# Performance work log

Hardware: AMD Instinct MI355X
Metric: run time of the kernel (lower is better)

Reference implementation:

```python
import jax, jax.numpy as jnp
import numpy as np

B, C, H, W = 4, 256, 64, 64
DQK = C // 4


def setup_inputs() -> dict:
    key = jax.random.key(0)
    ks = jax.random.split(key, 5)
    s = 0.05
    x = jax.random.normal(ks[0], (B, C, H, W), dtype=jnp.float32)
    Wq = jax.random.normal(ks[1], (DQK, C), dtype=jnp.float32) * s
    Wk = jax.random.normal(ks[2], (DQK, C), dtype=jnp.float32) * s
    Wv = jax.random.normal(ks[3], (C, C), dtype=jnp.float32) * s
    bq = jnp.zeros((DQK,), jnp.float32)
    bk = jnp.zeros((DQK,), jnp.float32)
    bv = jnp.zeros((C,), jnp.float32)
    gamma = jnp.zeros((1,), jnp.float32)
    return {"x": x, "Wq": Wq, "bq": bq, "Wk": Wk, "bk": bk,
            "Wv": Wv, "bv": bv, "gamma": gamma}


def reference(x, Wq, bq, Wk, bk, Wv, bv, gamma):
    b, c, h, w = x.shape
    n = h * w
    xf = x.reshape(b, c, n)                      # [B, C, N]
    # 1x1 convs == per-pixel linear projections
    q = jnp.einsum('dc,bcn->bnd', Wq, xf) + bq   # [B, N, Dqk]
    k = jnp.einsum('dc,bcn->bdn', Wk, xf) + bk[None, :, None]  # [B, Dqk, N]
    v = jnp.einsum('ec,bcn->ben', Wv, xf) + bv[None, :, None]  # [B, C, N]
    energy = jnp.einsum('bnd,bdm->bnm', q, k)    # [B, N, N]
    attn = jax.nn.softmax(energy, axis=-1)       # softmax over keys
    # out[b,c,i] = sum_j v[b,c,j] * attn[b,i,j]
    out = jnp.einsum('bcj,bij->bci', v, attn)    # [B, C, N]
    out = out.reshape(b, c, h, w)
    return gamma * out + x
```

## Files before the change

### kernel.cpp

```cpp
#include <hip/hip_runtime.h>

#define B_ 4
#define C_ 256
#define N_ 4096
#define D_ 64

typedef __bf16 bf16x8 __attribute__((ext_vector_type(8)));
typedef float floatx4 __attribute__((ext_vector_type(4)));
typedef float floatx16 __attribute__((ext_vector_type(16)));
typedef unsigned short ushort8v __attribute__((ext_vector_type(8)));
typedef unsigned short ushort4v __attribute__((ext_vector_type(4)));
typedef unsigned short ushort2v __attribute__((ext_vector_type(2)));

static __device__ __forceinline__ unsigned short f2bf(float f) {
    unsigned int u = __builtin_bit_cast(unsigned int, f);
    u += 0x7fffu + ((u >> 16) & 1u);
    return (unsigned short)(u >> 16);
}
static __device__ __forceinline__ float bf2f(unsigned short h) {
    unsigned int u = ((unsigned int)h) << 16;
    return __builtin_bit_cast(float, u);
}
static __device__ __forceinline__ unsigned int cvt_pk_bf16(float lo, float hi) {
    unsigned int d;
    asm("v_cvt_pk_bf16_f32 %0, %1, %2" : "=v"(d) : "v"(lo), "v"(hi));
    return d;
}

#define GLOAD16(gp, lp)                                                      \
    __builtin_amdgcn_global_load_lds(                                        \
        (const __attribute__((address_space(1))) void*)(gp),                 \
        (__attribute__((address_space(3))) void*)(lp), 16, 0, 0)

__global__ __launch_bounds__(256, 3) void proj_kernel(
    const float* __restrict__ x,
    const float* __restrict__ Wq, const float* __restrict__ Wk,
    const float* __restrict__ Wv,
    const float* __restrict__ bq, const float* __restrict__ bk,
    const float* __restrict__ bv,
    unsigned short* __restrict__ Qg, unsigned short* __restrict__ Kg,
    unsigned short* __restrict__ Vg)
{
    __shared__ __align__(16) unsigned short smem[64 * 264];
    unsigned short* xs = smem;
    unsigned short* Lt = smem;

    const int n0 = blockIdx.x * 64;
    const int f0 = blockIdx.y * 128;
    const int b  = blockIdx.z;
    const int t  = threadIdx.x;
    const int w  = t >> 6;
    const int lane = t & 63;
    const int g  = lane >> 4;
    const int m  = lane & 15;

#pragma unroll
    for (int k = 0; k < 8; ++k) {
        int e  = t + 256 * k;
        int cp = e >> 4;
        int c  = 2 * cp;
        int n4 = (e & 15) * 4;
        float4 v0 = *(const float4*)(x + ((size_t)b*C_ + c    )*N_ + n0 + n4);
        float4 v1 = *(const float4*)(x + ((size_t)b*C_ + c + 1)*N_ + n0 + n4);
        float a0[4] = {v0.x, v0.y, v0.z, v0.w};
        float a1[4] = {v1.x, v1.y, v1.z, v1.w};
#pragma unroll
        for (int j = 0; j < 4; ++j) {
            int n = n4 + j;
            unsigned int u = cvt_pk_bf16(a0[j], a1[j]);
            *(unsigned int*)&xs[n*264 + (((c >> 3) ^ (n & 7)) << 3) + (c & 7)] = u;
        }
    }

    float bias_[2][4];
#pragma unroll
    for (int mt = 0; mt < 2; ++mt)
#pragma unroll
        for (int r = 0; r < 4; ++r) {
            int fg = f0 + 32*w + 16*mt + 4*g + r;
            bias_[mt][r] = (fg < 64) ? bq[fg]
                         : (fg < 128) ? bk[fg - 64] : bv[fg - 128];
        }

    const int fr0 = f0 + 32*w + m;
    const int fr1 = fr0 + 16;
    const float* wr0 = (fr0 < 64) ? Wq + (size_t)fr0*C_
                     : (fr0 < 128)? Wk + (size_t)(fr0 - 64)*C_
                                  : Wv + (size_t)(fr0 - 128)*C_;
    const float* wr1 = (fr1 < 64) ? Wq + (size_t)fr1*C_
                     : (fr1 < 128)? Wk + (size_t)(fr1 - 64)*C_
                                  : Wv + (size_t)(fr1 - 128)*C_;
    bf16x8 afr[2][8];
#pragma unroll
    for (int ks = 0; ks < 8; ++ks) {
        float4 l0 = *(const float4*)(wr0 + 32*ks + 8*g);
        float4 h0 = *(const float4*)(wr0 + 32*ks + 8*g + 4);
        float4 l1 = *(const float4*)(wr1 + 32*ks + 8*g);
        float4 h1 = *(const float4*)(wr1 + 32*ks + 8*g + 4);
        uint4 u0, u1;
        u0.x = cvt_pk_bf16(l0.x, l0.y); u0.y = cvt_pk_bf16(l0.z, l0.w);
        u0.z = cvt_pk_bf16(h0.x, h0.y); u0.w = cvt_pk_bf16(h0.z, h0.w);
        u1.x = cvt_pk_bf16(l1.x, l1.y); u1.y = cvt_pk_bf16(l1.z, l1.w);
        u1.z = cvt_pk_bf16(h1.x, h1.y); u1.w = cvt_pk_bf16(h1.z, h1.w);
        afr[0][ks] = __builtin_bit_cast(bf16x8, u0);
        afr[1][ks] = __builtin_bit_cast(bf16x8, u1);
    }

    floatx4 acc[2][4];
#pragma unroll
    for (int mt = 0; mt < 2; ++mt)
#pragma unroll
        for (int nt = 0; nt < 4; ++nt) acc[mt][nt] = (floatx4){0.f,0.f,0.f,0.f};

    __syncthreads();

#pragma unroll
    for (int ks = 0; ks < 8; ++ks) {
#pragma unroll
        for (int nt = 0; nt < 4; ++nt) {
            int n = 16*nt + m;
            bf16x8 bfr = *(const bf16x8*)
                &xs[n*264 + (((4*ks + g) ^ (n & 7)) << 3)];
#pragma unroll
            for (int mt = 0; mt < 2; ++mt)
                acc[mt][nt] = __builtin_amdgcn_mfma_f32_16x16x32_bf16(
                                  afr[mt][ks], bfr, acc[mt][nt], 0, 0, 0);
        }
    }

    __syncthreads();

#pragma unroll
    for (int mt = 0; mt < 2; ++mt)
#pragma unroll
        for (int nt = 0; nt < 4; ++nt)
#pragma unroll
            for (int r = 0; r < 4; ++r)
                Lt[(32*w + 16*mt + 4*g + r)*72 + 16*nt + m] =
                    f2bf(acc[mt][nt][r] + bias_[mt][r]);
    __syncthreads();

    if (f0 == 0) {
#pragma unroll
        for (int k = 0; k < 4; ++k) {
            int e   = t + 256 * k;
            int fq0 = (e >> 6) * 8;
            int nl  = e & 63;
            ushort8v u;
#pragma unroll
            for (int j = 0; j < 8; ++j) u[j] = Lt[(fq0 + j)*72 + nl];
            unsigned short* dst = (fq0 < 64)
                ? (Qg + ((size_t)b*N_ + n0 + nl)*D_ + fq0)
                : (Kg + ((size_t)b*N_ + n0 + nl)*D_ + (fq0 - 64));
            *(ushort8v*)dst = u;
        }
    } else {
        const int cb = f0 - 128;
#pragma unroll
        for (int k = 0; k < 4; ++k) {
            int e  = t + 256 * k;
            int fr = e >> 3;
            int n8 = (e & 7) * 8;
            ushort8v u = *(const ushort8v*)&Lt[fr*72 + n8];
            *(ushort8v*)(Vg + ((size_t)b*C_ + cb + fr)*N_ + n0 + n8) = u;
        }
    }
}

__global__ __launch_bounds__(512, 2) void flash_kernel(
    const unsigned short* __restrict__ Qg, const unsigned short* __restrict__ Kg,
    const unsigned short* __restrict__ Vg,
    unsigned short* __restrict__ Opart, float* __restrict__ ML)
{
    __shared__ __align__(16) unsigned short Vlds[2][32 * 512];
    __shared__ __align__(16) unsigned short Klds[2][8 * 512];
    __shared__ float AL[8][32];

    const int gx   = blockIdx.x;
    const int tile = blockIdx.y;
    const int quarter = gx & 3;
    const int b    = gx >> 2;
    const int n0   = tile * 256;
    const int t    = threadIdx.x;
    const int w    = t >> 6;
    const int lane = t & 63;
    const int q32  = lane & 31;
    const int h    = lane >> 5;

    const unsigned short* Qb = Qg + ((size_t)b*N_ + n0)*D_;
    const unsigned short* Kb = Kg + (size_t)b*N_*D_;
    const unsigned short* Vb = Vg + (size_t)b*C_*N_;

    const int cstart = quarter * 16;
    const int cend   = cstart + 16;

    bf16x8 qf[4];
#pragma unroll
    for (int ks = 0; ks < 4; ++ks)
        qf[ks] = *(const bf16x8*)(Qb + (size_t)(32*w + q32)*D_ + 16*ks + 8*h);

    floatx16 accO[8];
#pragma unroll
    for (int ct = 0; ct < 8; ++ct)
#pragma unroll
        for (int r = 0; r < 16; ++r) accO[ct][r] = 0.f;

    float mrow = -1e30f, lrow = 0.f;

#define STAGE_K(T64, BUF) do {                                               \
    const unsigned short* gp = Kb                                            \
        + (size_t)((T64)*64 + 32*(w >> 2) + q32)*D_ + 16*(w & 3) + 8*h;      \
    GLOAD16(gp, &Klds[BUF][w * 512]); } while (0)

#define STAGE_V(T64, BUF) do {                                               \
    _Pragma("unroll")                                                        \
    for (int u_ = 0; u_ < 4; ++u_) {                                         \
        const unsigned short* gp = Vb                                        \
            + (size_t)(32*w + q32)*N_ + (T64)*64 + 16*u_ + 8*h;              \
        GLOAD16(gp, &Vlds[BUF][(w*4 + u_) * 512]);                           \
    } } while (0)

    STAGE_K(cstart, 0);
    STAGE_V(cstart, 0);
    __syncthreads();

    for (int t64 = cstart; t64 < cend; ++t64) {
        const int cur = (t64 - cstart) & 1;

        if (t64 + 1 < cend) {
            STAGE_K(t64 + 1, cur ^ 1);
            STAGE_V(t64 + 1, cur ^ 1);
        }

        floatx16 accS[2];
#pragma unroll
        for (int kt = 0; kt < 2; ++kt)
#pragma unroll
            for (int r = 0; r < 16; ++r) accS[kt][r] = 0.f;
#pragma unroll
        for (int kt = 0; kt < 2; ++kt)
#pragma unroll
            for (int ks = 0; ks < 4; ++ks) {
                bf16x8 kfr = *(const bf16x8*)
                    &Klds[cur][(kt*4 + ks)*512 + lane*8];
                accS[kt] = __builtin_amdgcn_mfma_f32_32x32x16_bf16(
                               kfr, qf[ks], accS[kt], 0, 0, 0);
            }

        float mx = -1e30f;
#pragma unroll
        for (int kt = 0; kt < 2; ++kt)
#pragma unroll
            for (int r = 0; r < 16; ++r) mx = fmaxf(mx, accS[kt][r]);
        mx = fmaxf(mx, __shfl_xor(mx, 32));
        float mnew  = fmaxf(mrow, mx);
        float alpha = __expf(mrow - mnew);
        mrow = mnew;
        float p[2][16];
        float rs = 0.f;
#pragma unroll
        for (int kt = 0; kt < 2; ++kt)
#pragma unroll
            for (int r = 0; r < 16; ++r) {
                float e = __expf(accS[kt][r] - mnew);
                p[kt][r] = e;
                rs += e;
            }
        rs += __shfl_xor(rs, 32);
        lrow = lrow * alpha + rs;
        if (h == 0) AL[w][q32] = alpha;

        bf16x8 pa[4];
#pragma unroll
        for (int kt = 0; kt < 2; ++kt)
#pragma unroll
            for (int cp = 0; cp < 2; ++cp) {
                unsigned int Y0 = cvt_pk_bf16(p[kt][8*cp + 0], p[kt][8*cp + 1]);
                unsigned int Y1 = cvt_pk_bf16(p[kt][8*cp + 2], p[kt][8*cp + 3]);
                unsigned int X0 = cvt_pk_bf16(p[kt][8*cp + 4], p[kt][8*cp + 5]);
                unsigned int X1 = cvt_pk_bf16(p[kt][8*cp + 6], p[kt][8*cp + 7]);
                asm volatile("v_permlane32_swap_b32 %0, %1"
                             : "+v"(Y0), "+v"(X0));
                asm volatile("v_permlane32_swap_b32 %0, %1"
                             : "+v"(Y1), "+v"(X1));
                uint4 fu; fu.x = Y0; fu.y = Y1; fu.z = X0; fu.w = X1;
                pa[kt*2 + cp] = __builtin_bit_cast(bf16x8, fu);
            }

        float4 av[4];
#pragma unroll
        for (int gp = 0; gp < 4; ++gp)
            av[gp] = *(const float4*)&AL[w][8*gp + 4*h];
#pragma unroll
        for (int ct = 0; ct < 8; ++ct)
#pragma unroll
            for (int gp = 0; gp < 4; ++gp)
#pragma unroll
                for (int i = 0; i < 4; ++i)
                    accO[ct][4*gp + i] *= av[gp][i];

        __builtin_amdgcn_s_setprio(1);
#pragma unroll
        for (int ct = 0; ct < 8; ++ct)
#pragma unroll
            for (int kc = 0; kc < 4; ++kc) {
                bf16x8 vf = *(const bf16x8*)
                    &Vlds[cur][(ct*4 + kc)*512 + lane*8];
                accO[ct] = __builtin_amdgcn_mfma_f32_32x32x16_bf16(
                               pa[kc], vf, accO[ct], 0, 0, 0);
            }
        __builtin_amdgcn_s_setprio(0);

        __syncthreads();
    }

    const size_t tbase = ((size_t)(quarter*B_ + b)*16 + tile);
    unsigned short* Ob = Opart + tbase * (C_ * 256);
    float* ml = ML + tbase * 512;

    if (h == 0) {
        ml[32*w + q32]       = mrow;
        ml[256 + 32*w + q32] = lrow;
    }

#pragma unroll
    for (int ct = 0; ct < 8; ++ct) {
        int c = 32*ct + q32;
#pragma unroll
        for (int gp = 0; gp < 4; ++gp) {
            uint2 pu;
            pu.x = cvt_pk_bf16(accO[ct][4*gp + 0], accO[ct][4*gp + 1]);
            pu.y = cvt_pk_bf16(accO[ct][4*gp + 2], accO[ct][4*gp + 3]);
            *(uint2*)(Ob + (size_t)c*256 + 32*w + 8*gp + 4*h) = pu;
        }
    }
#undef STAGE_K
#undef STAGE_V
}

__global__ __launch_bounds__(256) void combine_kernel(
    const unsigned short* __restrict__ Opart, const float* __restrict__ ML,
    const float* __restrict__ x, const float* __restrict__ gamma,
    float* __restrict__ out)
{
    __shared__ float sc[4][256];
    const int tile   = blockIdx.x;
    const int cslice = blockIdx.y;
    const int b      = blockIdx.z;
    const int n0     = tile * 256;
    const int t      = threadIdx.x;

    {
        float mm[4], ll[4];
        float M = -1e30f;
#pragma unroll
        for (int s = 0; s < 4; ++s) {
            const float* mls = ML + ((size_t)(s*B_ + b)*16 + tile)*512;
            mm[s] = mls[t];
            ll[s] = mls[256 + t];
            M = fmaxf(M, mm[s]);
        }
        float fs[4];
        float L = 0.f;
#pragma unroll
        for (int s = 0; s < 4; ++s) { fs[s] = __expf(mm[s] - M); L += fs[s]*ll[s]; }
        float gm = gamma[0];
#pragma unroll
        for (int s = 0; s < 4; ++s) sc[s][t] = gm * fs[s] / L;
    }
    __syncthreads();

    const int nq = t & 63;
    const int cl = t >> 6;
    const float* xb = x   + (size_t)b*C_*N_;
    float*       ob = out + (size_t)b*C_*N_;
    const unsigned short* Os[4];
#pragma unroll
    for (int s = 0; s < 4; ++s)
        Os[s] = Opart + ((size_t)(s*B_ + b)*16 + tile)*(C_*256);

    float sv[4][4];
#pragma unroll
    for (int s = 0; s < 4; ++s)
#pragma unroll
        for (int k = 0; k < 4; ++k) sv[s][k] = sc[s][4*nq + k];

#pragma unroll
    for (int i = 0; i < 8; ++i) {
        int c = 32*cslice + 4*i + cl;
        float4 x4 = *(const float4*)(xb + (size_t)c*N_ + n0 + 4*nq);
        float4 y = x4;
#pragma unroll
        for (int s = 0; s < 4; ++s) {
            ushort4v a4 = *(const ushort4v*)(Os[s] + (size_t)c*256 + 4*nq);
            y.x += sv[s][0]*bf2f(a4[0]);
            y.y += sv[s][1]*bf2f(a4[1]);
            y.z += sv[s][2]*bf2f(a4[2]);
            y.w += sv[s][3]*bf2f(a4[3]);
        }
        *(float4*)(ob + (size_t)c*N_ + n0 + 4*nq) = y;
    }
}

extern "C" void kernel_launch(void* const* d_in, const int* in_sizes, int n_in,
                              void* d_out, int out_size, void* d_ws, size_t ws_size,
                              hipStream_t stream) {
    const float* x     = (const float*)d_in[0];
    const float* Wq    = (const float*)d_in[1];
    const float* bq    = (const float*)d_in[2];
    const float* Wk    = (const float*)d_in[3];
    const float* bk    = (const float*)d_in[4];
    const float* Wv    = (const float*)d_in[5];
    const float* bv    = (const float*)d_in[6];
    const float* gamma = (const float*)d_in[7];
    float* out = (float*)d_out;

    unsigned short* Qg = (unsigned short*)d_ws;
    unsigned short* Kg = Qg + (size_t)B_*N_*D_;
    unsigned short* Vg = Kg + (size_t)B_*N_*D_;
    unsigned short* Op = Vg + (size_t)B_*C_*N_;
    float* ML = (float*)(Op + (size_t)4*B_*16*C_*256);

    proj_kernel<<<dim3(64, 3, 4), 256, 0, stream>>>(x, Wq, Wk, Wv,
                                                    bq, bk, bv, Qg, Kg, Vg);
    flash_kernel<<<dim3(16, 16), 512, 0, stream>>>(Qg, Kg, Vg, Op, ML);
    combine_kernel<<<dim3(16, 8, 4), 256, 0, stream>>>(Op, ML, x, gamma, out);
}
```

Measured before the change: 173.1 us.

## Software-pipeline PV MFMA one tile behind QK and skip unchanged-max rescale

The flash loop is restructured so the P·V MFMAs for the previous key tile run after the current tile's Q·K MFMAs, overlapping softmax math with matrix work. V gets a third LDS buffer so the previous tile stays resident while the next is prefetched. It also adds a lazy-rescale rule: if the new tile max exceeds the running max by no more than 8 across the whole wave, the max is left unchanged and the accumulator rescale is skipped. The cost is more LDS, which may lower occupancy at two blocks per CU, plus extra registers for the held-over P fragments and a small numerical risk from the bounded exponent growth.

```diff
diff --git a/kernel.cpp b/kernel.cpp
--- a/kernel.cpp
+++ b/kernel.cpp
@@ -172,7 +172,7 @@
     const unsigned short* __restrict__ Vg,
     unsigned short* __restrict__ Opart, float* __restrict__ ML)
 {
-    __shared__ __align__(16) unsigned short Vlds[2][32 * 512];
+    __shared__ __align__(16) unsigned short Vlds[3][32 * 512];
     __shared__ __align__(16) unsigned short Klds[2][8 * 512];
     __shared__ float AL[8][32];
 
@@ -206,6 +206,8 @@
         for (int r = 0; r < 16; ++r) accO[ct][r] = 0.f;
 
     float mrow = -1e30f, lrow = 0.f;
+    bf16x8 pa_prev[4];
+    bool skip_prev = true;
 
 #define STAGE_K(T64, BUF) do {                                               \
     const unsigned short* gp = Kb                                            \
@@ -220,99 +222,127 @@
         GLOAD16(gp, &Vlds[BUF][(w*4 + u_) * 512]);                           \
     } } while (0)
 
+#define FITER(T64, HASPV, HASPRE) do {                                       \
+    if (HASPRE) { STAGE_K((T64)+1, kcur ^ 1); STAGE_V((T64)+1, vnxt); }      \
+                                                          \
+    floatx16 accS[2];                                                        \
+    _Pragma("unroll")                                                        \
+    for (int kt = 0; kt < 2; ++kt)                                           \
+        _Pragma("unroll")                                                    \
+        for (int r = 0; r < 16; ++r) accS[kt][r] = 0.f;                      \
+    _Pragma("unroll")                                                        \
+    for (int kt = 0; kt < 2; ++kt)                                           \
+        _Pragma("unroll")                                                    \
+        for (int ks = 0; ks < 4; ++ks) {                                     \
+            bf16x8 kfr = *(const bf16x8*)                                    \
+                &Klds[kcur][(kt*4 + ks)*512 + lane*8];                       \
+            accS[kt] = __builtin_amdgcn_mfma_f32_32x32x16_bf16(              \
+                           kfr, qf[ks], accS[kt], 0, 0, 0);                  \
+        }                                                                    \
+                 \
+    if (HASPV) {                                                             \
+        if (!skip_prev) {                                                    \
+            float4 av_[4];                                                   \
+            _Pragma("unroll")                                                \
+            for (int gp_ = 0; gp_ < 4; ++gp_)                                \
+                av_[gp_] = *(const float4*)&AL[w][8*gp_ + 4*h];              \
+            _Pragma("unroll")                                                \
+            for (int ct = 0; ct < 8; ++ct)                                   \
+                _Pragma("unroll")                                            \
+                for (int gp_ = 0; gp_ < 4; ++gp_)                            \
+                    _Pragma("unroll")                                        \
+                    for (int i_ = 0; i_ < 4; ++i_)                           \
+                        accO[ct][4*gp_ + i_] *= av_[gp_][i_];                \
+        }                                                                    \
+        __builtin_amdgcn_s_setprio(1);                                       \
+        _Pragma("unroll")                                                    \
+        for (int ct = 0; ct < 8; ++ct)                                       \
+            _Pragma("unroll")                                                \
+            for (int kc = 0; kc < 4; ++kc) {                                 \
+                bf16x8 vf = *(const bf16x8*)                                 \
+                    &Vlds[vprv][(ct*4 + kc)*512 + lane*8];                   \
+                accO[ct] = __builtin_amdgcn_mfma_f32_32x32x16_bf16(          \
+                               pa_prev[kc], vf, accO[ct], 0, 0, 0);          \
+            }                                                                \
+        __builtin_amdgcn_s_setprio(0);                                       \
+    }                                                                        \
+                               \
+    float mx = -1e30f;                                                       \
+    _Pragma("unroll")                                                        \
+    for (int kt = 0; kt < 2; ++kt)                                           \
+        _Pragma("unroll")                                                    \
+        for (int r = 0; r < 16; ++r) mx = fmaxf(mx, accS[kt][r]);            \
+    mx = fmaxf(mx, __shfl_xor(mx, 32));                                      \
+    bool skip = __all(mx <= mrow + 8.f) != 0;                                \
+    float mnew  = skip ? mrow : fmaxf(mrow, mx);                             \
+    float alpha = __expf(mrow - mnew);                                       \
+    mrow = mnew;                                                             \
+    float p_[2][16];                                                         \
+    float rs = 0.f;                                                          \
+    _Pragma("unroll")                                                        \
+    for (int kt = 0; kt < 2; ++kt)                                           \
+        _Pragma("unroll")                                                    \
+        for (int r = 0; r < 16; ++r) {                                       \
+            float e_ = __expf(accS[kt][r] - mnew);                           \
+            p_[kt][r] = e_;                                                  \
+            rs += e_;                                                        \
+        }                                                                    \
+    rs += __shfl_xor(rs, 32);                                                \
+    lrow = lrow * alpha + rs;                                                \
+    if (!skip && h == 0) AL[w][q32] = alpha;                                 \
+    skip_prev = skip;                                                        \
+                      \
+    _Pragma("unroll")                                                        \
+    for (int kt = 0; kt < 2; ++kt)                                           \
+        _Pragma("unroll")                                                    \
+        for (int cp = 0; cp < 2; ++cp) {                                     \
+            unsigned int Y0 = cvt_pk_bf16(p_[kt][8*cp + 0], p_[kt][8*cp + 1]);\
+            unsigned int Y1 = cvt_pk_bf16(p_[kt][8*cp + 2], p_[kt][8*cp + 3]);\
+            unsigned int X0 = cvt_pk_bf16(p_[kt][8*cp + 4], p_[kt][8*cp + 5]);\
+            unsigned int X1 = cvt_pk_bf16(p_[kt][8*cp + 6], p_[kt][8*cp + 7]);\
+            asm volatile("v_permlane32_swap_b32 %0, %1" : "+v"(Y0), "+v"(X0));\
+            asm volatile("v_permlane32_swap_b32 %0, %1" : "+v"(Y1), "+v"(X1));\
+            uint4 fu; fu.x = Y0; fu.y = Y1; fu.z = X0; fu.w = X1;            \
+            pa_prev[kt*2 + cp] = __builtin_bit_cast(bf16x8, fu);             \
+        }                                                                    \
+    __syncthreads();        \
+    vprv = vcur; vcur = vnxt; vnxt = (vnxt + 1 == 3) ? 0 : vnxt + 1;         \
+    kcur ^= 1;                                                               \
+} while (0)
+
     STAGE_K(cstart, 0);
     STAGE_V(cstart, 0);
     __syncthreads();
 
-    for (int t64 = cstart; t64 < cend; ++t64) {
-        const int cur = (t64 - cstart) & 1;
-
-        if (t64 + 1 < cend) {
-            STAGE_K(t64 + 1, cur ^ 1);
-            STAGE_V(t64 + 1, cur ^ 1);
-        }
-
-        floatx16 accS[2];
-#pragma unroll
-        for (int kt = 0; kt < 2; ++kt)
-#pragma unroll
-            for (int r = 0; r < 16; ++r) accS[kt][r] = 0.f;
-#pragma unroll
-        for (int kt = 0; kt < 2; ++kt)
-#pragma unroll
-            for (int ks = 0; ks < 4; ++ks) {
-                bf16x8 kfr = *(const bf16x8*)
-                    &Klds[cur][(kt*4 + ks)*512 + lane*8];
-                accS[kt] = __builtin_amdgcn_mfma_f32_32x32x16_bf16(
-                               kfr, qf[ks], accS[kt], 0, 0, 0);
-            }
-
-        float mx = -1e30f;
-#pragma unroll
-        for (int kt = 0; kt < 2; ++kt)
-#pragma unroll
-            for (int r = 0; r < 16; ++r) mx = fmaxf(mx, accS[kt][r]);
-        mx = fmaxf(mx, __shfl_xor(mx, 32));
-        float mnew  = fmaxf(mrow, mx);
-        float alpha = __expf(mrow - mnew);
-        mrow = mnew;
-        float p[2][16];
-        float rs = 0.f;
-#pragma unroll
-        for (int kt = 0; kt < 2; ++kt)
-#pragma unroll
-            for (int r = 0; r < 16; ++r) {
-                float e = __expf(accS[kt][r] - mnew);
-                p[kt][r] = e;
-                rs += e;
-            }
-        rs += __shfl_xor(rs, 32);
-        lrow = lrow * alpha + rs;
-        if (h == 0) AL[w][q32] = alpha;
-
-        bf16x8 pa[4];
-#pragma unroll
-        for (int kt = 0; kt < 2; ++kt)
-#pragma unroll
-            for (int cp = 0; cp < 2; ++cp) {
-                unsigned int Y0 = cvt_pk_bf16(p[kt][8*cp + 0], p[kt][8*cp + 1]);
-                unsigned int Y1 = cvt_pk_bf16(p[kt][8*cp + 2], p[kt][8*cp + 3]);
-                unsigned int X0 = cvt_pk_bf16(p[kt][8*cp + 4], p[kt][8*cp + 5]);
-                unsigned int X1 = cvt_pk_bf16(p[kt][8*cp + 6], p[kt][8*cp + 7]);
-                asm volatile("v_permlane32_swap_b32 %0, %1"
-                             : "+v"(Y0), "+v"(X0));
-                asm volatile("v_permlane32_swap_b32 %0, %1"
-                             : "+v"(Y1), "+v"(X1));
-                uint4 fu; fu.x = Y0; fu.y = Y1; fu.z = X0; fu.w = X1;
-                pa[kt*2 + cp] = __builtin_bit_cast(bf16x8, fu);
-            }
-
-        float4 av[4];
-#pragma unroll
-        for (int gp = 0; gp < 4; ++gp)
-            av[gp] = *(const float4*)&AL[w][8*gp + 4*h];
+    int vcur = 0, vnxt = 1, vprv = 2, kcur = 0;
+
+    FITER(cstart, 0, 1);
+    for (int t64 = cstart + 1; t64 < cend - 1; ++t64)
+        FITER(t64, 1, 1);
+    FITER(cend - 1, 1, 0);
+
+    if (!skip_prev) {
+        float4 av_[4];
+#pragma unroll
+        for (int gp_ = 0; gp_ < 4; ++gp_)
+            av_[gp_] = *(const float4*)&AL[w][8*gp_ + 4*h];
 #pragma unroll
         for (int ct = 0; ct < 8; ++ct)
 #pragma unroll
-            for (int gp = 0; gp < 4; ++gp)
-#pragma unroll
-                for (int i = 0; i < 4; ++i)
-                    accO[ct][4*gp + i] *= av[gp][i];
-
-        __builtin_amdgcn_s_setprio(1);
-#pragma unroll
-        for (int ct = 0; ct < 8; ++ct)
-#pragma unroll
-            for (int kc = 0; kc < 4; ++kc) {
-                bf16x8 vf = *(const bf16x8*)
-                    &Vlds[cur][(ct*4 + kc)*512 + lane*8];
-                accO[ct] = __builtin_amdgcn_mfma_f32_32x32x16_bf16(
-                               pa[kc], vf, accO[ct], 0, 0, 0);
-            }
-        __builtin_amdgcn_s_setprio(0);
-
-        __syncthreads();
-    }
+            for (int gp_ = 0; gp_ < 4; ++gp_)
+#pragma unroll
+                for (int i_ = 0; i_ < 4; ++i_)
+                    accO[ct][4*gp_ + i_] *= av_[gp_][i_];
+    }
+#pragma unroll
+    for (int ct = 0; ct < 8; ++ct)
+#pragma unroll
+        for (int kc = 0; kc < 4; ++kc) {
+            bf16x8 vf = *(const bf16x8*)
+                &Vlds[vprv][(ct*4 + kc)*512 + lane*8];
+            accO[ct] = __builtin_amdgcn_mfma_f32_32x32x16_bf16(
+                           pa_prev[kc], vf, accO[ct], 0, 0, 0);
+        }
 
     const size_t tbase = ((size_t)(quarter*B_ + b)*16 + tile);
     unsigned short* Ob = Opart + tbase * (C_ * 256);
@@ -334,6 +364,7 @@
             *(uint2*)(Ob + (size_t)c*256 + 32*w + 8*gp + 4*h) = pu;
         }
     }
+#undef FITER
 #undef STAGE_K
 #undef STAGE_V
 }
```

After: 169.7 us. 2.0% less time.
